# Performance work log

Measured on AMD Instinct MI355X. Metric: run time of the kernel, lower is better.

The kernel has to match this reference:

```python
import jax, jax.numpy as jnp
import numpy as np

N = 63001
F_IN = 512
F_OUT = 256
E = 2_000_000
LRELU_ALPHA = 0.2


def setup_inputs() -> dict:
    key = jax.random.key(0)
    ks = jax.random.split(key, 10)
    x = jax.random.normal(ks[0], (N, F_IN), dtype=jnp.float32)
    values = jax.random.uniform(ks[1], (E,), dtype=jnp.float32)
    edge_index = jax.random.randint(ks[2], (2, E), 0, N, dtype=jnp.int32)
    # learned params: conv1d kernel_size=1 == dense matmuls
    W = jax.random.normal(ks[3], (F_IN, F_OUT), dtype=jnp.float32) * (1.0 / np.sqrt(F_IN))
    a1 = jax.random.normal(ks[4], (F_OUT,), dtype=jnp.float32) * (1.0 / np.sqrt(F_OUT))
    b1 = jnp.zeros((), dtype=jnp.float32)
    a2 = jax.random.normal(ks[5], (F_OUT,), dtype=jnp.float32) * (1.0 / np.sqrt(F_OUT))
    b2 = jnp.zeros((), dtype=jnp.float32)
    b_out = jnp.zeros((F_OUT,), dtype=jnp.float32)
    return {"x": x, "values": values, "edge_index": edge_index,
            "W": W, "a1": a1, "b1": b1, "a2": a2, "b2": b2, "b_out": b_out}


def reference(x, values, edge_index, W, a1, b1, a2, b2, b_out):
    src = edge_index[0]  # row index i of sparse adjacency entry
    dst = edge_index[1]  # col index j

    # conv1d(kernel=1) projections == matmuls
    seq_fts = x @ W                      # [N, F_out]
    f1 = seq_fts @ a1 + b1               # [N]
    f2 = seq_fts @ a2 + b2               # [N]

    # edgewise logits: s_ij * f1_i + s_ij * f2_j  (sparse_add of two masked broadcasts)
    logits = values * (f1[src] + f2[dst])           # [E]
    logits = jax.nn.leaky_relu(logits, LRELU_ALPHA)

    # sparse row-wise softmax over edges grouped by src
    m = jax.ops.segment_max(logits, src, num_segments=N)   # [N]
    p = jnp.exp(logits - m[src])                            # [E]
    denom = jax.ops.segment_sum(p, src, num_segments=N)     # [N]
    coefs = p / denom[src]                                  # [E]

    # SPMM: out_i = sum_j coef_ij * seq_fts_j
    out = jnp.zeros((N, F_OUT), dtype=seq_fts.dtype)
    out = out.at[src].add(coefs[:, None] * seq_fts[dst])

    out = out + b_out                                       # bias_add
    return jax.nn.elu(out)
```

## Files before the change

### kernel.cpp

```cpp
#include <hip/hip_runtime.h>
#include <hip/hip_bf16.h>
#include <cstdint>
#include <cstddef>

#define FIN 512
#define FOUT 256
#define LRELU 0.2f

typedef __attribute__((ext_vector_type(8))) short bf16x8;
typedef __attribute__((ext_vector_type(8))) unsigned short u16x8;
typedef __attribute__((ext_vector_type(4))) float f32x4;
typedef _Float16 h16x2 __attribute__((ext_vector_type(2)));

#define PERM_LO 0x05040100u
#define PERM_HI 0x07060302u
#define ONE2H   0x3C003C00u

__device__ inline ushort f2bf(float f) {
    __hip_bfloat16 h = __float2bfloat16(f);
    union { __hip_bfloat16 h; ushort u; } c; c.h = h;
    return c.u;
}
__device__ inline ushort f2h(float f) {
    union { _Float16 h; ushort u; } c; c.h = (_Float16)f;
    return c.u;
}
__device__ inline h16x2 u2h2(uint32_t u) {
    union { uint32_t u; h16x2 h; } c; c.u = u;
    return c.h;
}
__device__ inline float hdot2(h16x2 pp, uint32_t sv, float acc) {
    return __builtin_amdgcn_fdot2(pp, u2h2(sv), acc, false);
}

__global__ void pos_kernel(const int* __restrict__ src, int* __restrict__ cnt,
                           ushort* __restrict__ pos, int E, int posBlks,
                           const float* __restrict__ W, ushort* __restrict__ WT)
{
    if ((int)blockIdx.x >= posBlks) {
        const int idx = ((int)blockIdx.x - posBlks) * 256 + threadIdx.x;
        if (idx < FIN * FOUT) {
            const int k = idx >> 8, n = idx & 255;
            WT[(size_t)n * FIN + k] = f2bf(W[(size_t)k * FOUT + n]);
        }
        return;
    }
    int i = (blockIdx.x * blockDim.x + threadIdx.x) * 4;
    if (i + 4 <= E) {
        const int4 s = *(const int4*)(src + i);
        ushort4 p;
        p.x = (ushort)atomicAdd(&cnt[s.x], 1);
        p.y = (ushort)atomicAdd(&cnt[s.y], 1);
        p.z = (ushort)atomicAdd(&cnt[s.z], 1);
        p.w = (ushort)atomicAdd(&cnt[s.w], 1);
        *(ushort4*)(pos + i) = p;
    } else {
        for (; i < E; ++i) pos[i] = (ushort)atomicAdd(&cnt[src[i]], 1);
    }
}

#define BM 128
#define BK 64
__global__ __launch_bounds__(512) void gemm_bf16(
    const float* __restrict__ A, const ushort* __restrict__ BT,
    ushort* __restrict__ Ch,
    const float* __restrict__ a1, const float* __restrict__ a2,
    const float* __restrict__ b1, const float* __restrict__ b2,
    float* __restrict__ f1, float* __restrict__ f2,
    int M)
{
    __shared__ ushort As[BM * BK];
    __shared__ ushort Bs[FOUT * BK];
    __shared__ float f1s[BM][2];
    __shared__ float f2s[BM][2];
    const int t = threadIdx.x;
    const int lane = t & 63, w = t >> 6;
    const int wm = w & 3, wn = w >> 2;
    const int brow = blockIdx.x * BM;

    f32x4 acc[2][8] = {};

    const int ar = t >> 2;
    const int ak = (t & 3) << 4;
    const int grow = brow + ar;
    const bool arow_ok = (grow < M);
    const float* aptr = A + (size_t)grow * FIN + ak;

    const int bcol8 = (lane >> 3);
    const int bslot = lane & 7;
    const int bcdat = bslot ^ (bcol8 & 7);

    f32x4 va0, va1, va2, va3;
    if (arow_ok) {
        const f32x4* p = (const f32x4*)aptr;
        va0 = __builtin_nontemporal_load(p + 0);
        va1 = __builtin_nontemporal_load(p + 1);
        va2 = __builtin_nontemporal_load(p + 2);
        va3 = __builtin_nontemporal_load(p + 3);
    } else {
        va0 = va1 = va2 = va3 = (f32x4)0.f;
    }

    for (int k0 = 0; k0 < FIN; k0 += BK) {
#pragma unroll
        for (int j = 0; j < 4; ++j) {
            const int grp = w * 4 + j;
            const int col = grp * 8 + bcol8;
            const ushort* gsrc = BT + (size_t)col * FIN + k0 + bcdat * 8;
            ushort* ldst = &Bs[grp * 512];
            __builtin_amdgcn_global_load_lds(
                (const __attribute__((address_space(1))) void*)gsrc,
                (__attribute__((address_space(3))) void*)ldst, 16, 0, 0);
        }
        {
            u16x8 w0, w1;
            w0[0]=f2bf(va0[0]); w0[1]=f2bf(va0[1]); w0[2]=f2bf(va0[2]); w0[3]=f2bf(va0[3]);
            w0[4]=f2bf(va1[0]); w0[5]=f2bf(va1[1]); w0[6]=f2bf(va1[2]); w0[7]=f2bf(va1[3]);
            w1[0]=f2bf(va2[0]); w1[1]=f2bf(va2[1]); w1[2]=f2bf(va2[2]); w1[3]=f2bf(va2[3]);
            w1[4]=f2bf(va3[0]); w1[5]=f2bf(va3[1]); w1[6]=f2bf(va3[2]); w1[7]=f2bf(va3[3]);
            const int c0 = ((ak >> 3) + 0) ^ (ar & 7);
            const int c1 = ((ak >> 3) + 1) ^ (ar & 7);
            *(u16x8*)(&As[ar * BK + (c0 << 3)]) = w0;
            *(u16x8*)(&As[ar * BK + (c1 << 3)]) = w1;
        }
        __syncthreads();

        if (k0 + BK < FIN) {
            if (arow_ok) {
                const f32x4* p = (const f32x4*)(aptr + k0 + BK);
                va0 = __builtin_nontemporal_load(p + 0);
                va1 = __builtin_nontemporal_load(p + 1);
                va2 = __builtin_nontemporal_load(p + 2);
                va3 = __builtin_nontemporal_load(p + 3);
            }
        }

#pragma unroll
        for (int kk = 0; kk < 2; ++kk) {
            const int kc = kk * 4 + (lane >> 4);
            bf16x8 af[2], bfr[8];
#pragma unroll
            for (int m = 0; m < 2; ++m) {
                const int row = wm * 32 + m * 16 + (lane & 15);
                af[m] = *(const bf16x8*)(&As[row * BK + ((kc ^ (row & 7)) << 3)]);
            }
#pragma unroll
            for (int n = 0; n < 8; ++n) {
                const int col = wn * 128 + n * 16 + (lane & 15);
                bfr[n] = *(const bf16x8*)(&Bs[col * BK + ((kc ^ (col & 7)) << 3)]);
            }
#pragma unroll
            for (int m = 0; m < 2; ++m)
#pragma unroll
                for (int n = 0; n < 8; ++n)
                    acc[m][n] = __builtin_amdgcn_mfma_f32_16x16x32_bf16(
                        af[m], bfr[n], acc[m][n], 0, 0, 0);
        }
        __syncthreads();
    }

    float a1c[8], a2c[8];
#pragma unroll
    for (int n = 0; n < 8; ++n) {
        const int col = wn * 128 + n * 16 + (lane & 15);
        a1c[n] = a1[col];
        a2c[n] = a2[col];
    }
    const int cbase = wn * 128 + (lane & 15);
#pragma unroll
    for (int m = 0; m < 2; ++m) {
#pragma unroll
        for (int reg = 0; reg < 4; ++reg) {
            const int rloc = wm * 32 + m * 16 + (lane >> 4) * 4 + reg;
            const int r = brow + rloc;
            float p1 = 0.f, p2 = 0.f;
#pragma unroll
            for (int n = 0; n < 8; ++n) {
                p1 += acc[m][n][reg] * a1c[n];
                p2 += acc[m][n][reg] * a2c[n];
            }
#pragma unroll
            for (int off = 1; off < 16; off <<= 1) {
                p1 += __shfl_xor(p1, off);
                p2 += __shfl_xor(p2, off);
            }
            if ((lane & 15) == 0) {
                f1s[rloc][wn] = p1;
                f2s[rloc][wn] = p2;
            }
            if (r < M) {
#pragma unroll
                for (int n = 0; n < 8; ++n)
                    Ch[(size_t)r * FOUT + cbase + n * 16] = f2h(acc[m][n][reg]);
            }
        }
    }
    __syncthreads();
    if (t < BM) {
        const int r = brow + t;
        if (r < M) {
            f1[r] = f1s[t][0] + f1s[t][1] + b1[0];
            f2[r] = f2s[t][0] + f2s[t][1] + b2[0];
        }
    }
}

__global__ __launch_bounds__(1024) void scan_blk(const int* __restrict__ cnt,
                                                 int* __restrict__ btot, int K)
{
    __shared__ int s[1024];
    const int t = threadIdx.x;
    const int idx = blockIdx.x * 1024 + t;
    s[t] = (idx < K) ? cnt[idx] : 0;
    __syncthreads();
    for (int off = 512; off; off >>= 1) {
        if (t < off) s[t] += s[t + off];
        __syncthreads();
    }
    if (t == 0) btot[blockIdx.x] = s[0];
}

__global__ __launch_bounds__(64) void scan_top(const int* __restrict__ btot,
                                               int* __restrict__ boff, int nb)
{
    const int t = threadIdx.x;
    const int mine = (t < nb) ? btot[t] : 0;
    int v = mine;
#pragma unroll
    for (int off = 1; off < 64; off <<= 1) {
        const int u = __shfl_up(v, off);
        if (t >= off) v += u;
    }
    if (t < nb) boff[t] = v - mine;
}

__global__ __launch_bounds__(1024) void scan_out(const int* __restrict__ cnt,
                                                 const int* __restrict__ boff,
                                                 int* __restrict__ koff, int K)
{
    __shared__ int s[1024];
    const int t = threadIdx.x;
    const int b = blockIdx.x;
    const int idx = b * 1024 + t;
    const int v = (idx < K) ? cnt[idx] : 0;
    s[t] = v;
    __syncthreads();
    for (int off = 1; off < 1024; off <<= 1) {
        const int u = (t >= off) ? s[t - off] : 0;
        __syncthreads();
        s[t] += u;
        __syncthreads();
    }
    if (idx < K)      koff[idx] = boff[b] + s[t] - v;
    if (idx == K - 1) koff[K]   = boff[b] + s[t];
}

__global__ void scatter_p(const int* __restrict__ src, const int* __restrict__ dst,
                          const float* __restrict__ values, const ushort* __restrict__ pos,
                          const float* __restrict__ f1, const float* __restrict__ f2,
                          const int* __restrict__ koff,
                          uint32_t* __restrict__ pd, int E)
{
    const int i = blockIdx.x * blockDim.x + threadIdx.x;
    if (i < E) {
        const int s = src[i];
        const int d = dst[i];
        float lg = values[i] * (f1[s] + f2[d]);
        lg = (lg > 0.f) ? lg : LRELU * lg;
        const float p = __expf(lg);
        const int slot = koff[s] + (int)pos[i];
        pd[slot] = ((uint32_t)d << 16) | (uint32_t)f2h(p);
    }
}

__global__ __launch_bounds__(256) void spmm_kernel(
    const ushort* __restrict__ seq,
    const uint32_t* __restrict__ pd,
    const int* __restrict__ koff, const float* __restrict__ b_out,
    float* __restrict__ out, int N)
{
    const int w = threadIdx.x >> 6, lane = threadIdx.x & 63;
    const int row = blockIdx.x * 4 + w;
    if (row >= N) return;
    const int start = __builtin_amdgcn_readfirstlane(koff[row]);
    const int end   = __builtin_amdgcn_readfirstlane(koff[row + 1]);

    const ushort* seql = seq + lane * 4;
    float acc0 = 0.f, acc1 = 0.f, acc2 = 0.f, acc3 = 0.f, den = 0.f;

    int t = start;
    for (; t + 8 <= end; t += 8) {
        uint32_t q[8];
#pragma unroll
        for (int j = 0; j < 8; ++j) q[j] = pd[t + j];
        uint2 s[8];
#pragma unroll
        for (int j = 0; j < 8; ++j)
            s[j] = *(const uint2*)(seql + (size_t)(q[j] >> 16) * FOUT);
#pragma unroll
        for (int j = 0; j < 8; j += 2) {
            const h16x2 pp = u2h2((q[j] & 0xffffu) | (q[j + 1] << 16));
            acc0 = hdot2(pp, __builtin_amdgcn_perm(s[j+1].x, s[j].x, PERM_LO), acc0);
            acc1 = hdot2(pp, __builtin_amdgcn_perm(s[j+1].x, s[j].x, PERM_HI), acc1);
            acc2 = hdot2(pp, __builtin_amdgcn_perm(s[j+1].y, s[j].y, PERM_LO), acc2);
            acc3 = hdot2(pp, __builtin_amdgcn_perm(s[j+1].y, s[j].y, PERM_HI), acc3);
            den  = hdot2(pp, ONE2H, den);
        }
    }
    for (; t + 2 <= end; t += 2) {
        const uint32_t q0 = pd[t], q1 = pd[t + 1];
        const uint2 s0 = *(const uint2*)(seql + (size_t)(q0 >> 16) * FOUT);
        const uint2 s1 = *(const uint2*)(seql + (size_t)(q1 >> 16) * FOUT);
        const h16x2 pp = u2h2((q0 & 0xffffu) | (q1 << 16));
        acc0 = hdot2(pp, __builtin_amdgcn_perm(s1.x, s0.x, PERM_LO), acc0);
        acc1 = hdot2(pp, __builtin_amdgcn_perm(s1.x, s0.x, PERM_HI), acc1);
        acc2 = hdot2(pp, __builtin_amdgcn_perm(s1.y, s0.y, PERM_LO), acc2);
        acc3 = hdot2(pp, __builtin_amdgcn_perm(s1.y, s0.y, PERM_HI), acc3);
        den  = hdot2(pp, ONE2H, den);
    }
    if (t < end) {
        const uint32_t q0 = pd[t];
        const uint2 s0 = *(const uint2*)(seql + (size_t)(q0 >> 16) * FOUT);
        const h16x2 pp = u2h2(q0 & 0xffffu);
        acc0 = hdot2(pp, __builtin_amdgcn_perm(s0.x, s0.x, PERM_LO), acc0);
        acc1 = hdot2(pp, __builtin_amdgcn_perm(s0.x, s0.x, PERM_HI), acc1);
        acc2 = hdot2(pp, __builtin_amdgcn_perm(s0.y, s0.y, PERM_LO), acc2);
        acc3 = hdot2(pp, __builtin_amdgcn_perm(s0.y, s0.y, PERM_HI), acc3);
        den  = hdot2(pp, ONE2H, den);
    }

    const float inv = (end > start) ? 1.f / den : 0.f;
    const float4 bo = *(const float4*)(b_out + lane * 4);
    f32x4 o;
    o[0] = acc0 * inv + bo.x;
    o[1] = acc1 * inv + bo.y;
    o[2] = acc2 * inv + bo.z;
    o[3] = acc3 * inv + bo.w;
    o[0] = (o[0] > 0.f) ? o[0] : expm1f(o[0]);
    o[1] = (o[1] > 0.f) ? o[1] : expm1f(o[1]);
    o[2] = (o[2] > 0.f) ? o[2] : expm1f(o[2]);
    o[3] = (o[3] > 0.f) ? o[3] : expm1f(o[3]);
    __builtin_nontemporal_store(o, (f32x4*)(out + (size_t)row * FOUT + lane * 4));
}

extern "C" void kernel_launch(void* const* d_in, const int* in_sizes, int n_in,
                              void* d_out, int out_size, void* d_ws, size_t ws_size,
                              hipStream_t stream)
{
    const float* x      = (const float*)d_in[0];
    const float* values = (const float*)d_in[1];
    const int*   ei     = (const int*)d_in[2];
    const float* W      = (const float*)d_in[3];
    const float* a1     = (const float*)d_in[4];
    const float* b1     = (const float*)d_in[5];
    const float* a2     = (const float*)d_in[6];
    const float* b2     = (const float*)d_in[7];
    const float* b_out  = (const float*)d_in[8];
    float* out = (float*)d_out;

    const int N = in_sizes[0] / FIN;
    const int E = in_sizes[1];
    const int* src = ei;
    const int* dst = ei + E;

    auto alignup = [](size_t v) { return (v + 255) & ~(size_t)255; };
    char* ws = (char*)d_ws;
    size_t off = 0;
    ushort*   seqh = (ushort*)(ws + off);   off = alignup(off + (size_t)N * FOUT * 2);
    ushort*   WT   = (ushort*)(ws + off);   off = alignup(off + (size_t)FIN * FOUT * 2);
    float*    f1   = (float*)(ws + off);    off = alignup(off + (size_t)N * 4);
    float*    f2   = (float*)(ws + off);    off = alignup(off + (size_t)N * 4);
    int*      cnt  = (int*)(ws + off);      off = alignup(off + (size_t)N * 4);
    int*      koff = (int*)(ws + off);      off = alignup(off + (size_t)(N + 1) * 4);
    int*      btot = (int*)(ws + off);      off = alignup(off + (size_t)64 * 4);
    int*      boff = (int*)(ws + off);      off = alignup(off + (size_t)64 * 4);
    ushort*   pos  = (ushort*)(ws + off);   off = alignup(off + (size_t)E * 2);
    uint32_t* pd   = (uint32_t*)(ws + off); off = alignup(off + (size_t)E * 4);
    (void)ws_size;

    const int nb = (N + 1023) / 1024;
    const int posBlks = (E / 4 + 255) / 256;
    const int prepBlks = (FIN * FOUT + 255) / 256;

    hipMemsetAsync(cnt, 0, (size_t)N * 4, stream);

    pos_kernel<<<posBlks + prepBlks, 256, 0, stream>>>(src, cnt, pos, E, posBlks, W, WT);
    scan_blk<<<nb, 1024, 0, stream>>>(cnt, btot, N);
    scan_top<<<1, 64, 0, stream>>>(btot, boff, nb);
    scan_out<<<nb, 1024, 0, stream>>>(cnt, boff, koff, N);

    gemm_bf16<<<(N + BM - 1) / BM, 512, 0, stream>>>(x, WT, seqh, a1, a2, b1, b2,
                                                     f1, f2, N);

    scatter_p<<<(E + 255) / 256, 256, 0, stream>>>(src, dst, values, pos, f1, f2,
                                                   koff, pd, E);

    spmm_kernel<<<(N + 3) / 4, 256, 0, stream>>>(seqh, pd, koff, b_out, out, N);
}
```

Measured before the change: 331.4 us.

## Fuse edge position counting into GEMM launch and fold memset into prep kernel

The cnt zeroing memset moves into the W-transpose prep kernel. The atomic per-edge position counting now runs as extra blocks inside the GEMM launch, so the memory- and atomic-bound counting can overlap with the compute-bound GEMM instead of running as a separate serialized step. This removes two launches. The trade-off is that the counting blocks share the GEMM's 512-thread launch configuration and LDS allocation, which may reduce their occupancy.

Measured after the change: 341.6 us. 1.03x slower.

```diff
diff --git a/kernel.cpp b/kernel.cpp
--- a/kernel.cpp
+++ b/kernel.cpp
@@ -33,46 +33,53 @@
     return __builtin_amdgcn_fdot2(pp, u2h2(sv), acc, false);
 }
 
-__global__ void pos_kernel(const int* __restrict__ src, int* __restrict__ cnt,
-                           ushort* __restrict__ pos, int E, int posBlks,
-                           const float* __restrict__ W, ushort* __restrict__ WT)
-{
-    if ((int)blockIdx.x >= posBlks) {
-        const int idx = ((int)blockIdx.x - posBlks) * 256 + threadIdx.x;
-        if (idx < FIN * FOUT) {
-            const int k = idx >> 8, n = idx & 255;
-            WT[(size_t)n * FIN + k] = f2bf(W[(size_t)k * FOUT + n]);
-        }
-        return;
-    }
-    int i = (blockIdx.x * blockDim.x + threadIdx.x) * 4;
-    if (i + 4 <= E) {
-        const int4 s = *(const int4*)(src + i);
-        ushort4 p;
-        p.x = (ushort)atomicAdd(&cnt[s.x], 1);
-        p.y = (ushort)atomicAdd(&cnt[s.y], 1);
-        p.z = (ushort)atomicAdd(&cnt[s.z], 1);
-        p.w = (ushort)atomicAdd(&cnt[s.w], 1);
-        *(ushort4*)(pos + i) = p;
+__global__ void prep_kernel(const float* __restrict__ W, ushort* __restrict__ WT,
+                            int* __restrict__ cnt, int N)
+{
+    const int b = blockIdx.x;
+    if (b < 512) {
+        const int idx = b * 256 + threadIdx.x;
+        const int k = idx >> 8, n = idx & 255;
+        WT[(size_t)n * FIN + k] = f2bf(W[(size_t)k * FOUT + n]);
     } else {
-        for (; i < E; ++i) pos[i] = (ushort)atomicAdd(&cnt[src[i]], 1);
+        const int idx = (b - 512) * 256 + threadIdx.x;
+        if (idx < N) cnt[idx] = 0;
     }
 }
 
 #define BM 128
 #define BK 64
-__global__ __launch_bounds__(512) void gemm_bf16(
+__global__ __launch_bounds__(512) void mega_kernel(
     const float* __restrict__ A, const ushort* __restrict__ BT,
     ushort* __restrict__ Ch,
     const float* __restrict__ a1, const float* __restrict__ a2,
     const float* __restrict__ b1, const float* __restrict__ b2,
     float* __restrict__ f1, float* __restrict__ f2,
-    int M)
+    int M,
+    const int* __restrict__ src, int* __restrict__ cnt,
+    ushort* __restrict__ pos, int E, int gemmBlks)
 {
     __shared__ ushort As[BM * BK];
     __shared__ ushort Bs[FOUT * BK];
     __shared__ float f1s[BM][2];
     __shared__ float f2s[BM][2];
+
+    if ((int)blockIdx.x >= gemmBlks) {
+        int i = (((int)blockIdx.x - gemmBlks) * 512 + (int)threadIdx.x) * 4;
+        if (i + 4 <= E) {
+            const int4 s = *(const int4*)(src + i);
+            ushort4 p;
+            p.x = (ushort)atomicAdd(&cnt[s.x], 1);
+            p.y = (ushort)atomicAdd(&cnt[s.y], 1);
+            p.z = (ushort)atomicAdd(&cnt[s.z], 1);
+            p.w = (ushort)atomicAdd(&cnt[s.w], 1);
+            *(ushort4*)(pos + i) = p;
+        } else {
+            for (; i < E; ++i) pos[i] = (ushort)atomicAdd(&cnt[src[i]], 1);
+        }
+        return;
+    }
+
     const int t = threadIdx.x;
     const int lane = t & 63, w = t >> 6;
     const int wm = w & 3, wn = w >> 2;
@@ -379,19 +386,19 @@
     (void)ws_size;
 
     const int nb = (N + 1023) / 1024;
-    const int posBlks = (E / 4 + 255) / 256;
-    const int prepBlks = (FIN * FOUT + 255) / 256;
-
-    hipMemsetAsync(cnt, 0, (size_t)N * 4, stream);
-
-    pos_kernel<<<posBlks + prepBlks, 256, 0, stream>>>(src, cnt, pos, E, posBlks, W, WT);
+    const int zeroBlks = (N + 255) / 256;
+    const int gemmBlks = (N + BM - 1) / BM;
+    const int posBlks  = (E + 2047) / 2048;
+
+    prep_kernel<<<512 + zeroBlks, 256, 0, stream>>>(W, WT, cnt, N);
+
+    mega_kernel<<<gemmBlks + posBlks, 512, 0, stream>>>(
+        x, WT, seqh, a1, a2, b1, b2, f1, f2, N, src, cnt, pos, E, gemmBlks);
+
     scan_blk<<<nb, 1024, 0, stream>>>(cnt, btot, N);
     scan_top<<<1, 64, 0, stream>>>(btot, boff, nb);
     scan_out<<<nb, 1024, 0, stream>>>(cnt, boff, koff, N);
 
-    gemm_bf16<<<(N + BM - 1) / BM, 512, 0, stream>>>(x, WT, seqh, a1, a2, b1, b2,
-                                                     f1, f2, N);
-
     scatter_p<<<(E + 255) / 256, 256, 0, stream>>>(src, dst, values, pos, f1, f2,
                                                    koff, pd, E);
 
```

## Replicate per-row edge counters eight ways to cut atomic contention

Applied to the files above, without the earlier changes.

The per-source-row counter array is split into 8 replicas, chosen by thread group, so the atomics in the counting pass are spread over more addresses. The prefix scan now runs over N*8 interleaved entries, and the top-level scan is widened to a 1024-thread shared-memory scan to handle the larger block count. The scatter and SpMM kernels index koff with a stride of 8 so each replica keeps its own slot range within a row. This costs an 8x larger counter memset and a longer scan.

After: 328.7 us, median of 2. About the same (-0.8%).

```diff
diff --git a/kernel.cpp b/kernel.cpp
--- a/kernel.cpp
+++ b/kernel.cpp
@@ -6,6 +6,7 @@
 #define FIN 512
 #define FOUT 256
 #define LRELU 0.2f
+#define NREP 8
 
 typedef __attribute__((ext_vector_type(8))) short bf16x8;
 typedef __attribute__((ext_vector_type(8))) unsigned short u16x8;
@@ -34,7 +35,7 @@
 }
 
 __global__ void pos_kernel(const int* __restrict__ src, int* __restrict__ cnt,
-                           ushort* __restrict__ pos, int E, int posBlks,
+                           ushort* __restrict__ pos, int E, int N, int posBlks,
                            const float* __restrict__ W, ushort* __restrict__ WT)
 {
     if ((int)blockIdx.x >= posBlks) {
@@ -45,17 +46,20 @@
         }
         return;
     }
-    int i = (blockIdx.x * blockDim.x + threadIdx.x) * 4;
+    const int tg = blockIdx.x * blockDim.x + threadIdx.x;
+    const int rbase = (tg & 7) * N;
+    int i = tg * 4;
     if (i + 4 <= E) {
         const int4 s = *(const int4*)(src + i);
         ushort4 p;
-        p.x = (ushort)atomicAdd(&cnt[s.x], 1);
-        p.y = (ushort)atomicAdd(&cnt[s.y], 1);
-        p.z = (ushort)atomicAdd(&cnt[s.z], 1);
-        p.w = (ushort)atomicAdd(&cnt[s.w], 1);
+        p.x = (ushort)atomicAdd(&cnt[rbase + s.x], 1);
+        p.y = (ushort)atomicAdd(&cnt[rbase + s.y], 1);
+        p.z = (ushort)atomicAdd(&cnt[rbase + s.z], 1);
+        p.w = (ushort)atomicAdd(&cnt[rbase + s.w], 1);
         *(ushort4*)(pos + i) = p;
     } else {
-        for (; i < E; ++i) pos[i] = (ushort)atomicAdd(&cnt[src[i]], 1);
+        for (; i < E; ++i)
+            pos[i] = (ushort)atomicAdd(&cnt[((i >> 2) & 7) * N + src[i]], 1);
     }
 }
 
@@ -206,12 +210,12 @@
 }
 
 __global__ __launch_bounds__(1024) void scan_blk(const int* __restrict__ cnt,
-                                                 int* __restrict__ btot, int K)
+                                                 int* __restrict__ btot, int K, int N)
 {
     __shared__ int s[1024];
     const int t = threadIdx.x;
     const int idx = blockIdx.x * 1024 + t;
-    s[t] = (idx < K) ? cnt[idx] : 0;
+    s[t] = (idx < K) ? cnt[(idx & 7) * N + (idx >> 3)] : 0;
     __syncthreads();
     for (int off = 512; off; off >>= 1) {
         if (t < off) s[t] += s[t + off];
@@ -220,29 +224,32 @@
     if (t == 0) btot[blockIdx.x] = s[0];
 }
 
-__global__ __launch_bounds__(64) void scan_top(const int* __restrict__ btot,
-                                               int* __restrict__ boff, int nb)
-{
+__global__ __launch_bounds__(1024) void scan_top(const int* __restrict__ btot,
+                                                 int* __restrict__ boff, int nb)
+{
+    __shared__ int s[1024];
     const int t = threadIdx.x;
     const int mine = (t < nb) ? btot[t] : 0;
-    int v = mine;
-#pragma unroll
-    for (int off = 1; off < 64; off <<= 1) {
-        const int u = __shfl_up(v, off);
-        if (t >= off) v += u;
-    }
-    if (t < nb) boff[t] = v - mine;
+    s[t] = mine;
+    __syncthreads();
+    for (int off = 1; off < 1024; off <<= 1) {
+        const int u = (t >= off) ? s[t - off] : 0;
+        __syncthreads();
+        s[t] += u;
+        __syncthreads();
+    }
+    if (t < nb) boff[t] = s[t] - mine;
 }
 
 __global__ __launch_bounds__(1024) void scan_out(const int* __restrict__ cnt,
                                                  const int* __restrict__ boff,
-                                                 int* __restrict__ koff, int K)
+                                                 int* __restrict__ koff, int K, int N)
 {
     __shared__ int s[1024];
     const int t = threadIdx.x;
     const int b = blockIdx.x;
     const int idx = b * 1024 + t;
-    const int v = (idx < K) ? cnt[idx] : 0;
+    const int v = (idx < K) ? cnt[(idx & 7) * N + (idx >> 3)] : 0;
     s[t] = v;
     __syncthreads();
     for (int off = 1; off < 1024; off <<= 1) {
@@ -268,7 +275,7 @@
         float lg = values[i] * (f1[s] + f2[d]);
         lg = (lg > 0.f) ? lg : LRELU * lg;
         const float p = __expf(lg);
-        const int slot = koff[s] + (int)pos[i];
+        const int slot = koff[s * 8 + ((i >> 2) & 7)] + (int)pos[i];
         pd[slot] = ((uint32_t)d << 16) | (uint32_t)f2h(p);
     }
 }
@@ -282,8 +289,8 @@
     const int w = threadIdx.x >> 6, lane = threadIdx.x & 63;
     const int row = blockIdx.x * 4 + w;
     if (row >= N) return;
-    const int start = __builtin_amdgcn_readfirstlane(koff[row]);
-    const int end   = __builtin_amdgcn_readfirstlane(koff[row + 1]);
+    const int start = __builtin_amdgcn_readfirstlane(koff[row * 8]);
+    const int end   = __builtin_amdgcn_readfirstlane(koff[row * 8 + 8]);
 
     const ushort* seql = seq + lane * 4;
     float acc0 = 0.f, acc1 = 0.f, acc2 = 0.f, acc3 = 0.f, den = 0.f;
@@ -362,6 +369,7 @@
     const int E = in_sizes[1];
     const int* src = ei;
     const int* dst = ei + E;
+    const int K = N * NREP;
 
     auto alignup = [](size_t v) { return (v + 255) & ~(size_t)255; };
     char* ws = (char*)d_ws;
@@ -370,24 +378,24 @@
     ushort*   WT   = (ushort*)(ws + off);   off = alignup(off + (size_t)FIN * FOUT * 2);
     float*    f1   = (float*)(ws + off);    off = alignup(off + (size_t)N * 4);
     float*    f2   = (float*)(ws + off);    off = alignup(off + (size_t)N * 4);
-    int*      cnt  = (int*)(ws + off);      off = alignup(off + (size_t)N * 4);
-    int*      koff = (int*)(ws + off);      off = alignup(off + (size_t)(N + 1) * 4);
-    int*      btot = (int*)(ws + off);      off = alignup(off + (size_t)64 * 4);
-    int*      boff = (int*)(ws + off);      off = alignup(off + (size_t)64 * 4);
+    int*      cnt  = (int*)(ws + off);      off = alignup(off + (size_t)K * 4);
+    int*      koff = (int*)(ws + off);      off = alignup(off + (size_t)(K + 1) * 4);
+    int*      btot = (int*)(ws + off);      off = alignup(off + (size_t)1024 * 4);
+    int*      boff = (int*)(ws + off);      off = alignup(off + (size_t)1024 * 4);
     ushort*   pos  = (ushort*)(ws + off);   off = alignup(off + (size_t)E * 2);
     uint32_t* pd   = (uint32_t*)(ws + off); off = alignup(off + (size_t)E * 4);
     (void)ws_size;
 
-    const int nb = (N + 1023) / 1024;
+    const int nbk = (K + 1023) / 1024;
     const int posBlks = (E / 4 + 255) / 256;
     const int prepBlks = (FIN * FOUT + 255) / 256;
 
-    hipMemsetAsync(cnt, 0, (size_t)N * 4, stream);
-
-    pos_kernel<<<posBlks + prepBlks, 256, 0, stream>>>(src, cnt, pos, E, posBlks, W, WT);
-    scan_blk<<<nb, 1024, 0, stream>>>(cnt, btot, N);
-    scan_top<<<1, 64, 0, stream>>>(btot, boff, nb);
-    scan_out<<<nb, 1024, 0, stream>>>(cnt, boff, koff, N);
+    hipMemsetAsync(cnt, 0, (size_t)K * 4, stream);
+
+    pos_kernel<<<posBlks + prepBlks, 256, 0, stream>>>(src, cnt, pos, E, N, posBlks, W, WT);
+    scan_blk<<<nbk, 1024, 0, stream>>>(cnt, btot, K, N);
+    scan_top<<<1, 1024, 0, stream>>>(btot, boff, nbk);
+    scan_out<<<nbk, 1024, 0, stream>>>(cnt, boff, koff, K, N);
 
     gemm_bf16<<<(N + BM - 1) / BM, 512, 0, stream>>>(x, WT, seqh, a1, a2, b1, b2,
                                                      f1, f2, N);
```
